# Optimization experiments

Measured on AMD Instinct MI355X. Metric: run time of the kernel, lower is better.

The kernel has to match this reference:

```python
import jax, jax.numpy as jnp
import numpy as np
import math

B, S, D, H = 4, 512, 1024, 16
DH = D // H
DQ = D // 4
MIN_STEPS, MAX_STEPS = 4, 12
THR = 1e-4


def lin(t, w, b):
    # torch Linear convention: w is (out, in)
    return jnp.einsum('...i,oi->...o', t, w) + b


def gelu(t):
    return jax.nn.gelu(t, approximate=False)  # torch nn.GELU() exact


def layernorm(t, g, b):
    m = t.mean(-1, keepdims=True)
    v = jnp.mean(jnp.square(t - m), axis=-1, keepdims=True)
    return (t - m) * jax.lax.rsqrt(v + 1e-5) * g + b


def _forward(h, x, ig_w1, ig_b1, ig_w2, ig_b2, wq, bq, wk, bk, wv, bv, wo, bo,
             g1_w1, g1_b1, g1_w2, g1_b2, gate_logits, ln_g, ln_b,
             sp_w1, sp_b1, sp_w2, sp_b2):
    # adaptive step count: steps = base + floor(sigmoid(MLP(mean_pool(h))).mean() * extra)
    pooled = h.mean(axis=1)  # (B, D)
    extra = jax.nn.sigmoid(lin(gelu(lin(pooled, sp_w1, sp_b1)), sp_w2, sp_b2)).mean()
    num_steps = jnp.minimum(
        MIN_STEPS + jnp.floor(extra * (MAX_STEPS - MIN_STEPS)).astype(jnp.int32), MAX_STEPS)

    gw = jax.nn.softmax(gate_logits)  # gate weights over the 3 gates
    scale = 1.0 / math.sqrt(DH)

    def step(carry, i):
        h, active = carry
        # G1 gate (G2/G3 multiply zero memory/expert outputs -> drop)
        G1 = jax.nn.sigmoid(lin(gelu(lin(h, g1_w1, g1_b1)), g1_w2, g1_b2)) * gw[0]
        # Phi: input-gated blend + raw multi-head self-attention
        gate = jax.nn.sigmoid(
            lin(gelu(lin(jnp.concatenate([h, x], axis=-1), ig_w1, ig_b1)), ig_w2, ig_b2))
        blended = gate * h + (1.0 - gate) * x
        q = lin(blended, wq, bq).reshape(B, S, H, DH)
        k = lin(blended, wk, bk).reshape(B, S, H, DH)
        v = lin(blended, wv, bv).reshape(B, S, H, DH)
        attn = jax.nn.softmax(jnp.einsum('bqhd,bkhd->bhqk', q, k) * scale, axis=-1)
        ctx = jnp.einsum('bhqk,bkhd->bqhd', attn, v).reshape(B, S, D)
        phi = lin(ctx, wo, bo)
        h_new = layernorm(h + G1 * phi, ln_g, ln_b)
        res = jnp.linalg.norm(h_new - h) / (jnp.linalg.norm(h) + 1e-8)
        act_i = active & (i < num_steps)
        h = jnp.where(act_i, h_new, h)
        active = act_i & jnp.logical_not((i >= MIN_STEPS) & (res < THR))
        return (h, active), None

    (h, _), _ = jax.lax.scan(step, (h, jnp.array(True)), jnp.arange(MAX_STEPS))
    return h


def setup_inputs() -> dict:
    key = jax.random.key(0)
    ks = jax.random.split(key, 16)
    f32 = jnp.float32

    def W(k, out_d, in_d):
        return jax.random.normal(k, (out_d, in_d), f32) * (1.0 / np.sqrt(in_d))

    return {
        'h': jax.random.normal(ks[0], (B, S, D), f32),
        'x': jax.random.normal(ks[1], (B, S, D), f32),
        # PhiLayer input_gate: Linear(2D, D/4) -> GELU -> Linear(D/4, D) -> Sigmoid
        'ig_w1': W(ks[2], DQ, 2 * D), 'ig_b1': jnp.zeros((DQ,), f32),
        'ig_w2': W(ks[3], D, DQ), 'ig_b2': jnp.zeros((D,), f32),
        # QKV / out projections (xavier-ish, zero bias)
        'wq': W(ks[4], D, D), 'bq': jnp.zeros((D,), f32),
        'wk': W(ks[5], D, D), 'bk': jnp.zeros((D,), f32),
        'wv': W(ks[6], D, D), 'bv': jnp.zeros((D,), f32),
        'wo': W(ks[7], D, D), 'bo': jnp.zeros((D,), f32),
        # Gating gate #1 MLP (only G1 contributes; memory/experts are zero)
        'g1_w1': W(ks[8], DQ, D), 'g1_b1': jnp.zeros((DQ,), f32),
        'g1_w2': W(ks[9], D, DQ), 'g1_b2': jnp.zeros((D,), f32),
        'gate_logits': jnp.ones((3,), f32),  # nn.Parameter(torch.ones(3))
        # LayerNorm
        'ln_g': jnp.ones((D,), f32), 'ln_b': jnp.zeros((D,), f32),
        # step predictor: Linear(D, D/4) -> GELU -> Linear(D/4, 1)
        'sp_w1': W(ks[10], DQ, D), 'sp_b1': jnp.zeros((DQ,), f32),
        'sp_w2': W(ks[11], 1, DQ), 'sp_b2': jnp.zeros((1,), f32),
    }


def reference(h, x, ig_w1, ig_b1, ig_w2, ig_b2, wq, bq, wk, bk, wv, bv, wo, bo,
              g1_w1, g1_b1, g1_w2, g1_b2, gate_logits, ln_g, ln_b,
              sp_w1, sp_b1, sp_w2, sp_b2):
    return _forward(h, x, ig_w1, ig_b1, ig_w2, ig_b2, wq, bq, wk, bk, wv, bv, wo, bo,
                    g1_w1, g1_b1, g1_w2, g1_b2, gate_logits, ln_g, ln_b,
                    sp_w1, sp_b1, sp_w2, sp_b2)
```

## Files before the change

### kernel.cpp

```cpp
#include <hip/hip_runtime.h>
#include <hip/hip_bf16.h>


#define B_   4
#define S_   512
#define D_   1024
#define H_   16
#define DH_  64
#define MSEQ 2048

typedef short short8 __attribute__((ext_vector_type(8)));
typedef float floatx4 __attribute__((ext_vector_type(4)));

static constexpr size_t OFF_H    = 0;
static constexpr size_t OFF_X    = 2097152;
static constexpr size_t OFF_HXB  = 4194304;
static constexpr size_t OFF_T2B  = 6291456;
static constexpr size_t OFF_T1B  = 6553600;
static constexpr size_t OFF_G1B  = 6815744;
static constexpr size_t OFF_QKVB = 7864320;
static constexpr size_t OFF_U    = 7864320;
static constexpr size_t OFF_CTXB = 11010048;
static constexpr size_t OFF_WARE = 12058624;
static constexpr size_t OFF_BIAS = 14811136;
static constexpr size_t OFF_POOL = 14817792;
static constexpr size_t OFF_SPT  = 14821888;
static constexpr size_t OFF_PPART= 14822912;
static constexpr size_t OFF_SCAL = 14888448;

static constexpr int W_WIG1 = 0;
static constexpr int W_WIG2 = 524288;
static constexpr int W_WG1  = 786432;
static constexpr int W_WG2  = 1048576;
static constexpr int W_QKV  = 1310720;
static constexpr int W_WO   = 4456448;
static constexpr int W_TOT  = 5505024;
static constexpr int B_TOT  = 6656;

__device__ __forceinline__ float bf2f(unsigned int u) {
  return __uint_as_float((u & 0xFFFFu) << 16);
}
__device__ __forceinline__ short f2bs(float f) {
  __hip_bfloat16 b = __float2bfloat16(f);
  return *reinterpret_cast<short*>(&b);
}
__device__ __forceinline__ unsigned int pk2(float lo, float hi) {
  return (unsigned int)(unsigned short)f2bs(lo) | ((unsigned int)(unsigned short)f2bs(hi) << 16);
}
__device__ __forceinline__ float ldf(const void* p, size_t i, int f32m) {
  return f32m ? ((const float*)p)[i] : bf2f(((const unsigned short*)p)[i]);
}
__device__ __forceinline__ float gelu_f(float x) {
  return 0.5f * x * (1.0f + erff(x * 0.70710678118654752440f));
}
__device__ __forceinline__ float sig_f(float x) {
  return 1.0f / (1.0f + expf(-x));
}
__device__ __forceinline__ void gl_lds16(const short* gp, short* lp) {
  __builtin_amdgcn_global_load_lds(
      (const __attribute__((address_space(1))) unsigned int*)gp,
      (__attribute__((address_space(3))) unsigned int*)lp, 16, 0, 0);
}
__device__ __forceinline__ float wave_sum(float v) {
  #pragma unroll
  for (int off = 32; off > 0; off >>= 1) v += __shfl_xor(v, off);
  return v;
}

__global__ void detect_kernel(const void* ln_g, int* dtf) {
  *dtf = (((const unsigned int*)ln_g)[0] == 0x3F800000u) ? 1 : 0;
}

struct RepackPtrs {
  const void* w[8];
  const void* b[8];
};

__global__ __launch_bounds__(256) void repack_all_kernel(
    const int* __restrict__ dtf, RepackPtrs ps,
    short* __restrict__ wdst, float* __restrict__ bdst) {
  const int f32m = *dtf;
  int i = blockIdx.x * 256 + threadIdx.x;
  if (i < W_TOT) {
    const int off[9] = {0, 524288, 786432, 1048576, 1310720, 2359296, 3407872, 4456448, W_TOT};
    int seg = 0;
    #pragma unroll
    for (int s = 1; s < 8; s++) seg += (i >= off[s]) ? 1 : 0;
    wdst[i] = f2bs(ldf(ps.w[seg], i - off[seg], f32m));
  } else if (i < W_TOT + B_TOT) {
    int j = i - W_TOT;
    const int off[9] = {0, 256, 1280, 1536, 2560, 3584, 4608, 5632, B_TOT};
    int seg = 0;
    #pragma unroll
    for (int s = 1; s < 8; s++) seg += (j >= off[s]) ? 1 : 0;
    bdst[j] = ldf(ps.b[seg], j - off[seg], f32m);
  }
}

__global__ __launch_bounds__(256) void cvt_in_kernel(
    const int* __restrict__ dtf, const void* __restrict__ hb,
    const void* __restrict__ xb, float* __restrict__ h, float* __restrict__ x,
    short* __restrict__ hxb, int n) {
  int f32m = *dtf;
  int i = blockIdx.x * 256 + threadIdx.x;
  if (i < n) {
    float hv = ldf(hb, i, f32m);
    float xv = ldf(xb, i, f32m);
    h[i] = hv;
    x[i] = xv;
    int row = i >> 10, col = i & 1023;
    hxb[(size_t)row * 2048 + col] = f2bs(hv);
    hxb[(size_t)row * 2048 + 1024 + col] = f2bs(xv);
  }
}

__global__ __launch_bounds__(256) void cvt_out_kernel(
    const int* __restrict__ dtf, const float* __restrict__ h, void* __restrict__ out, int n) {
  int f32m = *dtf;
  int i = blockIdx.x * 256 + threadIdx.x;
  if (i < n) {
    if (f32m) ((float*)out)[i] = h[i];
    else ((__hip_bfloat16*)out)[i] = __float2bfloat16(h[i]);
  }
}

__global__ __launch_bounds__(256) void pool_s1_kernel(
    const float* __restrict__ H, float* __restrict__ part) {
  int b = blockIdx.x, c = blockIdx.y, tid = threadIdx.x;
  const float* p = H + ((size_t)b * S_ + c * 32) * D_;
  #pragma unroll
  for (int rep = 0; rep < 4; rep++) {
    int d = rep * 256 + tid;
    float s = 0.f;
    for (int r = 0; r < 32; r++) s += p[(size_t)r * D_ + d];
    part[((size_t)b * 16 + c) * D_ + d] = s;
  }
}
__global__ __launch_bounds__(256) void pool_s2_kernel(
    const float* __restrict__ part, float* __restrict__ pooled) {
  int i = blockIdx.x * 256 + threadIdx.x;
  int b = i >> 10, d = i & 1023;
  float s = 0.f;
  #pragma unroll
  for (int c = 0; c < 16; c++) s += part[((size_t)b * 16 + c) * D_ + d];
  pooled[i] = s * (1.0f / (float)S_);
}

__device__ __forceinline__ float blk_sum256(float v, float* sm, int tid) {
  #pragma unroll
  for (int off = 32; off > 0; off >>= 1) v += __shfl_xor(v, off);
  __syncthreads();
  if ((tid & 63) == 0) sm[tid >> 6] = v;
  __syncthreads();
  return sm[0] + sm[1] + sm[2] + sm[3];
}

__global__ __launch_bounds__(256) void sp1_kernel(
    const int* __restrict__ dtf, const float* __restrict__ pooled,
    const void* __restrict__ w1, const void* __restrict__ b1,
    float* __restrict__ spt) {
  __shared__ float sm[4];
  const int f32m = *dtf;
  int j = blockIdx.x, tid = threadIdx.x;
  float s[4] = {0.f, 0.f, 0.f, 0.f};
  #pragma unroll
  for (int r = 0; r < 4; r++) {
    int k = tid * 4 + r;
    float w = ldf(w1, (size_t)j * D_ + k, f32m);
    s[0] += pooled[k] * w;
    s[1] += pooled[1024 + k] * w;
    s[2] += pooled[2048 + k] * w;
    s[3] += pooled[3072 + k] * w;
  }
  #pragma unroll
  for (int b = 0; b < 4; b++) {
    float t = blk_sum256(s[b], sm, tid);
    __syncthreads();
    if (tid == 0) spt[b * 256 + j] = gelu_f(t + ldf(b1, j, f32m));
  }
}

__global__ __launch_bounds__(256) void sp2_kernel(
    const int* __restrict__ dtf, const float* __restrict__ spt,
    const void* __restrict__ w2, const void* __restrict__ b2,
    const void* __restrict__ glog,
    int* __restrict__ num_steps, int* __restrict__ active, int* __restrict__ cur,
    float* __restrict__ gw0, float* __restrict__ ssd, float* __restrict__ ssh,
    int* __restrict__ cnt) {
  __shared__ float z[4];
  const int f32m = *dtf;
  int tid = threadIdx.x;
  if (tid < 12) cnt[tid] = 0;
  int wave = tid >> 6, lane = tid & 63;
  {
    int b = wave;
    float s = spt[b * 256 + lane]       * ldf(w2, lane, f32m) +
              spt[b * 256 + lane + 64]  * ldf(w2, lane + 64, f32m) +
              spt[b * 256 + lane + 128] * ldf(w2, lane + 128, f32m) +
              spt[b * 256 + lane + 192] * ldf(w2, lane + 192, f32m);
    #pragma unroll
    for (int off = 32; off > 0; off >>= 1) s += __shfl_xor(s, off);
    if (lane == 0) z[b] = sig_f(s + ldf(b2, 0, f32m));
  }
  __syncthreads();
  if (tid == 0) {
    float extra = 0.25f * (z[0] + z[1] + z[2] + z[3]);
    int ns = 4 + (int)floorf(extra * 8.0f);
    if (ns > 12) ns = 12;
    *num_steps = ns;
    *active = 1;
    *cur = 1;
    *ssd = 0.f; *ssh = 0.f;
    float g0 = ldf(glog, 0, f32m);
    float g1 = ldf(glog, 1, f32m);
    float g2 = ldf(glog, 2, f32m);
    float mx = fmaxf(g0, fmaxf(g1, g2));
    float e0 = expf(g0 - mx), e1 = expf(g1 - mx), e2 = expf(g2 - mx);
    *gw0 = e0 / (e0 + e1 + e2);
  }
}

enum { EPI_NONE = 0, EPI_GELU = 1, EPI_SIGSCALE = 2, EPI_BLEND = 3, EPI_RESADD = 4 };

template <int EPI, int BM, int BN>
__device__ __forceinline__ void mgemm_core(
    short* As, short* Bs,
    const short* __restrict__ A, int lda,
    const short* __restrict__ W, const float* __restrict__ bias, int K, int N,
    float* __restrict__ Cf, short* __restrict__ Cb,
    const float* __restrict__ aux1, const float* __restrict__ aux2f,
    const short* __restrict__ aux2b, const float* __restrict__ scale_ptr,
    int m0, int n0) {
  constexpr int FM = (BM / 2) / 16;
  constexpr int FN = (BN / 2) / 16;
  constexpr int CPA = (BM / 16) / 4;
  constexpr int CPB = (BN / 16) / 4;
  const int tid = threadIdx.x;
  const int lane = tid & 63, wv_ = tid >> 6;
  const int wm = (wv_ >> 1) * (BM / 2), wn = (wv_ & 1) * (BN / 2);
  const int srow = lane >> 2, scol = (lane & 3) * 8;
  const int frow = lane & 15, fk = (lane >> 4) * 8;

  floatx4 acc[FM][FN];
  #pragma unroll
  for (int i = 0; i < FM; i++)
    #pragma unroll
    for (int j = 0; j < FN; j++) acc[i][j] = (floatx4){0.f, 0.f, 0.f, 0.f};

  for (int k0 = 0; k0 < K; k0 += 64) {
    __syncthreads();
    #pragma unroll
    for (int c = 0; c < CPA; c++) {
      int q = wv_ * CPA + c;
      const short* gp = A + (size_t)(m0 + q * 16 + srow) * lda + k0 + scol;
      gl_lds16(gp, As + q * 512);
      gl_lds16(gp + 32, As + BM * 32 + q * 512);
    }
    #pragma unroll
    for (int c = 0; c < CPB; c++) {
      int q = wv_ * CPB + c;
      const short* gp = W + (size_t)(n0 + q * 16 + srow) * K + k0 + scol;
      gl_lds16(gp, Bs + q * 512);
      gl_lds16(gp + 32, Bs + BN * 32 + q * 512);
    }
    __syncthreads();
    #pragma unroll
    for (int hlf = 0; hlf < 2; hlf++) {
      const short* Ah = As + hlf * BM * 32;
      const short* Bh = Bs + hlf * BN * 32;
      short8 a[FM], b[FN];
      #pragma unroll
      for (int i = 0; i < FM; i++)
        a[i] = *reinterpret_cast<const short8*>(&Ah[(wm + i * 16 + frow) * 32 + fk]);
      #pragma unroll
      for (int j = 0; j < FN; j++)
        b[j] = *reinterpret_cast<const short8*>(&Bh[(wn + j * 16 + frow) * 32 + fk]);
      #pragma unroll
      for (int i = 0; i < FM; i++)
        #pragma unroll
        for (int j = 0; j < FN; j++)
          acc[i][j] = __builtin_amdgcn_mfma_f32_16x16x32_bf16(a[i], b[j], acc[i][j], 0, 0, 0);
    }
  }

  float gwv = 0.f;
  if (EPI == EPI_SIGSCALE) gwv = *scale_ptr;
  const int rq = (lane >> 4) * 4;
  #pragma unroll
  for (int i = 0; i < FM; i++) {
    #pragma unroll
    for (int j = 0; j < FN; j++) {
      int n = n0 + wn + j * 16 + (lane & 15);
      float bv = bias[n];
      #pragma unroll
      for (int r = 0; r < 4; r++) {
        int m = m0 + wm + i * 16 + rq + r;
        size_t off = (size_t)m * N + n;
        float v = acc[i][j][r] + bv;
        if (EPI == EPI_GELU) {
          Cb[off] = f2bs(gelu_f(v));
        } else if (EPI == EPI_SIGSCALE) {
          Cb[off] = f2bs(sig_f(v) * gwv);
        } else if (EPI == EPI_BLEND) {
          float s = sig_f(v);
          Cb[off] = f2bs(s * aux1[off] + (1.f - s) * aux2f[off]);
        } else if (EPI == EPI_RESADD) {
          Cf[off] = aux1[off] + bf2f((unsigned short)aux2b[off]) * v;
        } else {
          Cb[off] = f2bs(v);
        }
      }
    }
  }
}

template <int EPI, int BM, int BN>
__global__ __launch_bounds__(256) void mgemm(
    const int* __restrict__ flag, const short* __restrict__ A, int lda,
    const short* __restrict__ W, const float* __restrict__ bias, int K, int N,
    float* __restrict__ Cf, short* __restrict__ Cb,
    const float* __restrict__ aux1, const float* __restrict__ aux2f,
    const short* __restrict__ aux2b, const float* __restrict__ scale_ptr) {
  if (*flag == 0) return;
  __shared__ short As[BM * 64];
  __shared__ short Bs[BN * 64];
  mgemm_core<EPI, BM, BN>(As, Bs, A, lda, W, bias, K, N, Cf, Cb,
                          aux1, aux2f, aux2b, scale_ptr,
                          blockIdx.y * BM, blockIdx.x * BN);
}

__global__ __launch_bounds__(256) void gate1_kernel(
    const int* __restrict__ flag, const short* __restrict__ hxb,
    const short* __restrict__ warena, const float* __restrict__ biasA,
    short* __restrict__ t2b, short* __restrict__ t1b) {
  if (*flag == 0) return;
  __shared__ short As[64 * 64];
  __shared__ short Bs[64 * 64];
  if (blockIdx.z == 0)
    mgemm_core<EPI_GELU, 64, 64>(As, Bs, hxb, 2048, warena + W_WIG1, biasA + 0,
                                 2048, 256, nullptr, t2b, nullptr, nullptr, nullptr,
                                 nullptr, blockIdx.y * 64, blockIdx.x * 64);
  else
    mgemm_core<EPI_GELU, 64, 64>(As, Bs, hxb, 2048, warena + W_WG1, biasA + 1280,
                                 1024, 256, nullptr, t1b, nullptr, nullptr, nullptr,
                                 nullptr, blockIdx.y * 64, blockIdx.x * 64);
}

__global__ __launch_bounds__(256) void gate2_kernel(
    const int* __restrict__ flag, const short* __restrict__ t2b,
    const short* __restrict__ t1b, const short* __restrict__ warena,
    const float* __restrict__ biasA, short* __restrict__ bldb,
    short* __restrict__ g1b, const float* __restrict__ h,
    const float* __restrict__ xf, const float* __restrict__ gw0) {
  if (*flag == 0) return;
  __shared__ short As[128 * 64];
  __shared__ short Bs[64 * 64];
  if (blockIdx.z == 0)
    mgemm_core<EPI_BLEND, 128, 64>(As, Bs, t2b, 256, warena + W_WIG2, biasA + 256,
                                   256, 1024, nullptr, bldb, h, xf, nullptr,
                                   nullptr, blockIdx.y * 128, blockIdx.x * 64);
  else
    mgemm_core<EPI_SIGSCALE, 128, 64>(As, Bs, t1b, 256, warena + W_WG2, biasA + 1536,
                                      256, 1024, nullptr, g1b, nullptr, nullptr,
                                      nullptr, gw0, blockIdx.y * 128, blockIdx.x * 64);
}

#define AP_ 72
__global__ __launch_bounds__(256) void attn_kernel(
    const int* __restrict__ flag, const short* __restrict__ qkv,
    short* __restrict__ ctxb) {
  if (*flag == 0) return;
  __shared__ short Ks[64 * AP_];
  __shared__ short Vt[64 * AP_];
  __shared__ short Ps[64 * AP_];
  const int tid = threadIdx.x;
  const int lane = tid & 63, wv = tid >> 6;
  const int ln15 = lane & 15, quad = lane >> 4;
  const int qt = blockIdx.x, hh = blockIdx.y, b = blockIdx.z;
  const int wm = wv * 16;
  const size_t rowbase = (size_t)b * S_;
  const int hcol = hh * DH_;
  const float scale = 0.125f;

  short8 qa[2];
  {
    const short* qp = qkv + (rowbase + qt * 64 + wm + ln15) * 3072 + hcol + quad * 8;
    qa[0] = *reinterpret_cast<const short8*>(qp);
    qa[1] = *reinterpret_cast<const short8*>(qp + 32);
  }
  const int skk = tid >> 2, scg = (tid & 3) * 16;

  float mrow[4] = {-1e30f, -1e30f, -1e30f, -1e30f};
  float lrow[4] = {0.f, 0.f, 0.f, 0.f};
  floatx4 accO[4];
  #pragma unroll
  for (int j = 0; j < 4; j++) accO[j] = (floatx4){0.f, 0.f, 0.f, 0.f};

  for (int kt = 0; kt < 8; kt++) {
    __syncthreads();
    {
      const short* gk = qkv + (rowbase + kt * 64 + skk) * 3072 + 1024 + hcol + scg;
      uint4 k0 = *reinterpret_cast<const uint4*>(gk);
      uint4 k1 = *reinterpret_cast<const uint4*>(gk + 8);
      *reinterpret_cast<uint4*>(&Ks[skk * AP_ + scg]) = k0;
      *reinterpret_cast<uint4*>(&Ks[skk * AP_ + scg + 8]) = k1;
      short8 v0 = *reinterpret_cast<const short8*>(gk + 1024);
      short8 v1 = *reinterpret_cast<const short8*>(gk + 1032);
      #pragma unroll
      for (int j = 0; j < 8; j++) Vt[(scg + j) * AP_ + skk] = v0[j];
      #pragma unroll
      for (int j = 0; j < 8; j++) Vt[(scg + 8 + j) * AP_ + skk] = v1[j];
    }
    __syncthreads();

    floatx4 sc[4];
    #pragma unroll
    for (int nf = 0; nf < 4; nf++) {
      short8 b0 = *reinterpret_cast<const short8*>(&Ks[(nf * 16 + ln15) * AP_ + quad * 8]);
      short8 b1 = *reinterpret_cast<const short8*>(&Ks[(nf * 16 + ln15) * AP_ + 32 + quad * 8]);
      floatx4 s = (floatx4){0.f, 0.f, 0.f, 0.f};
      s = __builtin_amdgcn_mfma_f32_16x16x32_bf16(qa[0], b0, s, 0, 0, 0);
      s = __builtin_amdgcn_mfma_f32_16x16x32_bf16(qa[1], b1, s, 0, 0, 0);
      sc[nf] = s;
    }

    float prob[4][4];
    #pragma unroll
    for (int r = 0; r < 4; r++) {
      float lm = fmaxf(fmaxf(sc[0][r], sc[1][r]), fmaxf(sc[2][r], sc[3][r])) * scale;
      lm = fmaxf(lm, __shfl_xor(lm, 1));
      lm = fmaxf(lm, __shfl_xor(lm, 2));
      lm = fmaxf(lm, __shfl_xor(lm, 4));
      lm = fmaxf(lm, __shfl_xor(lm, 8));
      float mn = fmaxf(mrow[r], lm);
      float alpha = expf(mrow[r] - mn);
      float ls = 0.f;
      #pragma unroll
      for (int nf = 0; nf < 4; nf++) {
        float p = expf(sc[nf][r] * scale - mn);
        prob[nf][r] = p;
        ls += p;
      }
      ls += __shfl_xor(ls, 1);
      ls += __shfl_xor(ls, 2);
      ls += __shfl_xor(ls, 4);
      ls += __shfl_xor(ls, 8);
      lrow[r] = lrow[r] * alpha + ls;
      mrow[r] = mn;
      #pragma unroll
      for (int df = 0; df < 4; df++) accO[df][r] *= alpha;
    }
    #pragma unroll
    for (int nf = 0; nf < 4; nf++)
      #pragma unroll
      for (int r = 0; r < 4; r++)
        Ps[(wm + quad * 4 + r) * AP_ + nf * 16 + ln15] = f2bs(prob[nf][r]);
    __syncthreads();

    short8 pa0 = *reinterpret_cast<const short8*>(&Ps[(wm + ln15) * AP_ + quad * 8]);
    short8 pa1 = *reinterpret_cast<const short8*>(&Ps[(wm + ln15) * AP_ + 32 + quad * 8]);
    #pragma unroll
    for (int df = 0; df < 4; df++) {
      short8 bv0 = *reinterpret_cast<const short8*>(&Vt[(df * 16 + ln15) * AP_ + quad * 8]);
      short8 bv1 = *reinterpret_cast<const short8*>(&Vt[(df * 16 + ln15) * AP_ + 32 + quad * 8]);
      accO[df] = __builtin_amdgcn_mfma_f32_16x16x32_bf16(pa0, bv0, accO[df], 0, 0, 0);
      accO[df] = __builtin_amdgcn_mfma_f32_16x16x32_bf16(pa1, bv1, accO[df], 0, 0, 0);
    }
  }

  float inv[4];
  #pragma unroll
  for (int r = 0; r < 4; r++) inv[r] = 1.0f / lrow[r];
  #pragma unroll
  for (int df = 0; df < 4; df++) {
    #pragma unroll
    for (int r = 0; r < 4; r++) {
      size_t off = (rowbase + qt * 64 + wm + quad * 4 + r) * 1024 + hcol + df * 16 + ln15;
      ctxb[off] = f2bs(accO[df][r] * inv[r]);
    }
  }
}

__global__ __launch_bounds__(256) void ln_kernel(
    int step_i, const int* __restrict__ flagp, const int* __restrict__ dtf,
    const float* __restrict__ U, float* __restrict__ H, short* __restrict__ hxb,
    const void* __restrict__ g, const void* __restrict__ be,
    float* __restrict__ ssd, float* __restrict__ ssh,
    int* __restrict__ active, int* __restrict__ cur,
    const int* __restrict__ num_steps, int* __restrict__ cnt) {
  const int flag = *flagp;
  const int f32m = *dtf;
  __shared__ float sdd[4], sdh[4];
  const int tid = threadIdx.x;
  const int wv = tid >> 6, lane = tid & 63;
  if (flag) {
    const int row = blockIdx.x * 4 + wv;
    const float4* u4 = reinterpret_cast<const float4*>(U + (size_t)row * D_);
    float4* h4 = reinterpret_cast<float4*>(H + (size_t)row * D_);
    float4 uv[4], hv[4];
    #pragma unroll
    for (int j = 0; j < 4; j++) uv[j] = u4[lane + 64 * j];
    #pragma unroll
    for (int j = 0; j < 4; j++) hv[j] = h4[lane + 64 * j];
    float s = 0.f;
    #pragma unroll
    for (int j = 0; j < 4; j++) s += (uv[j].x + uv[j].y) + (uv[j].z + uv[j].w);
    s = wave_sum(s);
    float mean = s * (1.0f / (float)D_);
    float4 d[4];
    float vv = 0.f;
    #pragma unroll
    for (int j = 0; j < 4; j++) {
      d[j].x = uv[j].x - mean; d[j].y = uv[j].y - mean;
      d[j].z = uv[j].z - mean; d[j].w = uv[j].w - mean;
      vv += d[j].x * d[j].x + d[j].y * d[j].y + d[j].z * d[j].z + d[j].w * d[j].w;
    }
    vv = wave_sum(vv);
    float rstd = rsqrtf(vv * (1.0f / (float)D_) + 1e-5f);
    float lsd = 0.f, lsh = 0.f;
    #pragma unroll
    for (int j = 0; j < 4; j++) {
      int c = (lane + 64 * j) * 4;
      float hn0 = d[j].x * rstd * ldf(g, c + 0, f32m) + ldf(be, c + 0, f32m);
      float hn1 = d[j].y * rstd * ldf(g, c + 1, f32m) + ldf(be, c + 1, f32m);
      float hn2 = d[j].z * rstd * ldf(g, c + 2, f32m) + ldf(be, c + 2, f32m);
      float hn3 = d[j].w * rstd * ldf(g, c + 3, f32m) + ldf(be, c + 3, f32m);
      float e0 = hn0 - hv[j].x, e1 = hn1 - hv[j].y, e2 = hn2 - hv[j].z, e3 = hn3 - hv[j].w;
      lsd += e0 * e0 + e1 * e1 + e2 * e2 + e3 * e3;
      lsh += hv[j].x * hv[j].x + hv[j].y * hv[j].y + hv[j].z * hv[j].z + hv[j].w * hv[j].w;
      h4[lane + 64 * j] = make_float4(hn0, hn1, hn2, hn3);
      uint2 pw;
      pw.x = pk2(hn0, hn1);
      pw.y = pk2(hn2, hn3);
      *reinterpret_cast<uint2*>(hxb + (size_t)row * 2048 + c) = pw;
    }
    lsd = wave_sum(lsd);
    lsh = wave_sum(lsh);
    if (lane == 0) { sdd[wv] = lsd; sdh[wv] = lsh; }
    __syncthreads();
    if (tid == 0) {
      atomicAdd(ssd, (sdd[0] + sdd[1]) + (sdd[2] + sdd[3]));
      atomicAdd(ssh, (sdh[0] + sdh[1]) + (sdh[2] + sdh[3]));
    }
  }
  if (tid == 0) {
    __threadfence();
    int old = atomicAdd(&cnt[step_i], 1);
    if (old == (int)gridDim.x - 1) {
      if (flag && step_i >= 4) {
        float nd = atomicAdd(ssd, 0.0f);
        float nh = atomicAdd(ssh, 0.0f);
        float res = sqrtf(nd) / (sqrtf(nh) + 1e-8f);
        if (res < 1e-4f) *active = 0;
      }
      *cur = ((*active) && (step_i + 1 < *num_steps)) ? 1 : 0;
      *ssd = 0.f; *ssh = 0.f;
    }
  }
}

extern "C" void kernel_launch(void* const* d_in, const int* in_sizes, int n_in,
                              void* d_out, int out_size, void* d_ws, size_t ws_size,
                              hipStream_t stream) {
  (void)in_sizes; (void)n_in; (void)out_size; (void)ws_size;
  const void* h_in  = d_in[0];
  const void* x_in  = d_in[1];
  const void* glog  = d_in[18];
  const void* ln_g  = d_in[19];
  const void* ln_b  = d_in[20];
  const void* sp_w1 = d_in[21];
  const void* sp_b1 = d_in[22];
  const void* sp_w2 = d_in[23];
  const void* sp_b2 = d_in[24];

  RepackPtrs rp;
  rp.w[0] = d_in[2];  rp.w[1] = d_in[4];  rp.w[2] = d_in[14]; rp.w[3] = d_in[16];
  rp.w[4] = d_in[6];  rp.w[5] = d_in[8];  rp.w[6] = d_in[10]; rp.w[7] = d_in[12];
  rp.b[0] = d_in[3];  rp.b[1] = d_in[5];  rp.b[2] = d_in[15]; rp.b[3] = d_in[17];
  rp.b[4] = d_in[7];  rp.b[5] = d_in[9];  rp.b[6] = d_in[11]; rp.b[7] = d_in[13];

  float* wsf = (float*)d_ws;
  float* h      = wsf + OFF_H;
  float* xf     = wsf + OFF_X;
  short* hxb    = (short*)(wsf + OFF_HXB);
  short* t2b    = (short*)(wsf + OFF_T2B);
  short* t1b    = (short*)(wsf + OFF_T1B);
  short* g1b    = (short*)(wsf + OFF_G1B);
  short* qkvb   = (short*)(wsf + OFF_QKVB);
  float* u      = wsf + OFF_U;
  short* ctxb   = (short*)(wsf + OFF_CTXB);
  short* bldb   = ctxb;
  short* warena = (short*)(wsf + OFF_WARE);
  float* biasA  = wsf + OFF_BIAS;
  float* pooled = wsf + OFF_POOL;
  float* spt    = wsf + OFF_SPT;
  float* ppart  = wsf + OFF_PPART;
  float* ssd    = wsf + OFF_SCAL + 0;
  float* ssh    = wsf + OFF_SCAL + 1;
  float* gw0    = wsf + OFF_SCAL + 2;
  int* ip        = (int*)(wsf + OFF_SCAL + 8);
  int* num_steps = ip + 0;
  int* active    = ip + 1;
  int* cur       = ip + 2;
  int* dtf       = ip + 3;
  int* cnt       = ip + 4;

  const int NTOT = B_ * S_ * D_;

  detect_kernel<<<1, 1, 0, stream>>>(ln_g, dtf);
  repack_all_kernel<<<(W_TOT + B_TOT + 255) / 256, 256, 0, stream>>>(dtf, rp, warena, biasA);
  cvt_in_kernel<<<NTOT / 256, 256, 0, stream>>>(dtf, h_in, x_in, h, xf, hxb, NTOT);
  pool_s1_kernel<<<dim3(4, 16), 256, 0, stream>>>(h, ppart);
  pool_s2_kernel<<<16, 256, 0, stream>>>(ppart, pooled);
  sp1_kernel<<<256, 256, 0, stream>>>(dtf, pooled, sp_w1, sp_b1, spt);
  sp2_kernel<<<1, 256, 0, stream>>>(dtf, spt, sp_w2, sp_b2, glog,
                                    num_steps, active, cur, gw0, ssd, ssh, cnt);
  for (int i = 0; i < 12; i++) {
    gate1_kernel<<<dim3(4, 32, 2), 256, 0, stream>>>(cur, hxb, warena, biasA, t2b, t1b);
    gate2_kernel<<<dim3(16, 16, 2), 256, 0, stream>>>(cur, t2b, t1b, warena, biasA,
                                                      bldb, g1b, h, xf, gw0);
    mgemm<EPI_NONE, 128, 64><<<dim3(48, 16), 256, 0, stream>>>(
        cur, bldb, 1024, warena + W_QKV, biasA + 2560, 1024, 3072,
        nullptr, qkvb, nullptr, nullptr, nullptr, nullptr);
    attn_kernel<<<dim3(8, 16, 4), 256, 0, stream>>>(cur, qkvb, ctxb);
    mgemm<EPI_RESADD, 128, 64><<<dim3(16, 16), 256, 0, stream>>>(
        cur, ctxb, 1024, warena + W_WO, biasA + 5632, 1024, 1024,
        u, nullptr, h, nullptr, g1b, nullptr);
    ln_kernel<<<512, 256, 0, stream>>>(i, cur, dtf, u, h, hxb, ln_g, ln_b,
                                       ssd, ssh, active, cur, num_steps, cnt);
  }
  cvt_out_kernel<<<NTOT / 256, 256, 0, stream>>>(dtf, h, (void*)d_out, NTOT);
}
```

Baseline: 1.275 ms.

## Fuse per-step kernels into persistent megakernel with grid barriers and early exit

Replaces the 12-iteration loop of six kernel launches per step (gate1, gate2, QKV GEMM, attention, output GEMM, layernorm) with one persistent kernel of 512 blocks. The stages are separated by a software grid barrier built on an atomic counter, and the kernel breaks out of the loop once the step count or convergence test says to stop. This removes launch overhead and the no-op launches that ran after convergence, and the output conversion is folded into the kernel's tail. The cost is spin-wait barriers, which only work if all 512 blocks are co-resident and would deadlock otherwise. Per-step residual accumulators replace reset logic, and stages with fewer work items than blocks leave some blocks idle.

After: 3.858 ms. 203% more time.

```diff
diff --git a/kernel.cpp b/kernel.cpp
--- a/kernel.cpp
+++ b/kernel.cpp
@@ -8,6 +8,7 @@
 #define H_   16
 #define DH_  64
 #define MSEQ 2048
+#define NBLK 512
 
 typedef short short8 __attribute__((ext_vector_type(8)));
 typedef float floatx4 __attribute__((ext_vector_type(4)));
@@ -67,6 +68,20 @@
   return v;
 }
 
+__device__ __forceinline__ void gbar(int* bar, int& nbar) {
+  __syncthreads();
+  if (threadIdx.x == 0) {
+    __threadfence();
+    __hip_atomic_fetch_add(bar, 1, __ATOMIC_RELAXED, __HIP_MEMORY_SCOPE_AGENT);
+    const int target = NBLK * (nbar + 1);
+    while (__hip_atomic_load(bar, __ATOMIC_RELAXED, __HIP_MEMORY_SCOPE_AGENT) < target)
+      __builtin_amdgcn_s_sleep(2);
+    __threadfence();
+  }
+  __syncthreads();
+  nbar++;
+}
+
 __global__ void detect_kernel(const void* ln_g, int* dtf) {
   *dtf = (((const unsigned int*)ln_g)[0] == 0x3F800000u) ? 1 : 0;
 }
@@ -114,16 +129,6 @@
   }
 }
 
-__global__ __launch_bounds__(256) void cvt_out_kernel(
-    const int* __restrict__ dtf, const float* __restrict__ h, void* __restrict__ out, int n) {
-  int f32m = *dtf;
-  int i = blockIdx.x * 256 + threadIdx.x;
-  if (i < n) {
-    if (f32m) ((float*)out)[i] = h[i];
-    else ((__hip_bfloat16*)out)[i] = __float2bfloat16(h[i]);
-  }
-}
-
 __global__ __launch_bounds__(256) void pool_s1_kernel(
     const float* __restrict__ H, float* __restrict__ part) {
   int b = blockIdx.x, c = blockIdx.y, tid = threadIdx.x;
@@ -184,13 +189,13 @@
     const int* __restrict__ dtf, const float* __restrict__ spt,
     const void* __restrict__ w2, const void* __restrict__ b2,
     const void* __restrict__ glog,
-    int* __restrict__ num_steps, int* __restrict__ active, int* __restrict__ cur,
-    float* __restrict__ gw0, float* __restrict__ ssd, float* __restrict__ ssh,
-    int* __restrict__ cnt) {
+    int* __restrict__ num_steps, float* __restrict__ gw0,
+    float* __restrict__ ssdA, float* __restrict__ sshA, int* __restrict__ bar) {
   __shared__ float z[4];
   const int f32m = *dtf;
   int tid = threadIdx.x;
-  if (tid < 12) cnt[tid] = 0;
+  if (tid < 12) { ssdA[tid] = 0.f; sshA[tid] = 0.f; }
+  if (tid == 16) *bar = 0;
   int wave = tid >> 6, lane = tid & 63;
   {
     int b = wave;
@@ -208,9 +213,6 @@
     int ns = 4 + (int)floorf(extra * 8.0f);
     if (ns > 12) ns = 12;
     *num_steps = ns;
-    *active = 1;
-    *cur = 1;
-    *ssd = 0.f; *ssh = 0.f;
     float g0 = ldf(glog, 0, f32m);
     float g1 = ldf(glog, 1, f32m);
     float g2 = ldf(glog, 2, f32m);
@@ -314,69 +316,16 @@
   }
 }
 
-template <int EPI, int BM, int BN>
-__global__ __launch_bounds__(256) void mgemm(
-    const int* __restrict__ flag, const short* __restrict__ A, int lda,
-    const short* __restrict__ W, const float* __restrict__ bias, int K, int N,
-    float* __restrict__ Cf, short* __restrict__ Cb,
-    const float* __restrict__ aux1, const float* __restrict__ aux2f,
-    const short* __restrict__ aux2b, const float* __restrict__ scale_ptr) {
-  if (*flag == 0) return;
-  __shared__ short As[BM * 64];
-  __shared__ short Bs[BN * 64];
-  mgemm_core<EPI, BM, BN>(As, Bs, A, lda, W, bias, K, N, Cf, Cb,
-                          aux1, aux2f, aux2b, scale_ptr,
-                          blockIdx.y * BM, blockIdx.x * BN);
-}
-
-__global__ __launch_bounds__(256) void gate1_kernel(
-    const int* __restrict__ flag, const short* __restrict__ hxb,
-    const short* __restrict__ warena, const float* __restrict__ biasA,
-    short* __restrict__ t2b, short* __restrict__ t1b) {
-  if (*flag == 0) return;
-  __shared__ short As[64 * 64];
-  __shared__ short Bs[64 * 64];
-  if (blockIdx.z == 0)
-    mgemm_core<EPI_GELU, 64, 64>(As, Bs, hxb, 2048, warena + W_WIG1, biasA + 0,
-                                 2048, 256, nullptr, t2b, nullptr, nullptr, nullptr,
-                                 nullptr, blockIdx.y * 64, blockIdx.x * 64);
-  else
-    mgemm_core<EPI_GELU, 64, 64>(As, Bs, hxb, 2048, warena + W_WG1, biasA + 1280,
-                                 1024, 256, nullptr, t1b, nullptr, nullptr, nullptr,
-                                 nullptr, blockIdx.y * 64, blockIdx.x * 64);
-}
-
-__global__ __launch_bounds__(256) void gate2_kernel(
-    const int* __restrict__ flag, const short* __restrict__ t2b,
-    const short* __restrict__ t1b, const short* __restrict__ warena,
-    const float* __restrict__ biasA, short* __restrict__ bldb,
-    short* __restrict__ g1b, const float* __restrict__ h,
-    const float* __restrict__ xf, const float* __restrict__ gw0) {
-  if (*flag == 0) return;
-  __shared__ short As[128 * 64];
-  __shared__ short Bs[64 * 64];
-  if (blockIdx.z == 0)
-    mgemm_core<EPI_BLEND, 128, 64>(As, Bs, t2b, 256, warena + W_WIG2, biasA + 256,
-                                   256, 1024, nullptr, bldb, h, xf, nullptr,
-                                   nullptr, blockIdx.y * 128, blockIdx.x * 64);
-  else
-    mgemm_core<EPI_SIGSCALE, 128, 64>(As, Bs, t1b, 256, warena + W_WG2, biasA + 1536,
-                                      256, 1024, nullptr, g1b, nullptr, nullptr,
-                                      nullptr, gw0, blockIdx.y * 128, blockIdx.x * 64);
-}
-
 #define AP_ 72
-__global__ __launch_bounds__(256) void attn_kernel(
-    const int* __restrict__ flag, const short* __restrict__ qkv,
-    short* __restrict__ ctxb) {
-  if (*flag == 0) return;
-  __shared__ short Ks[64 * AP_];
-  __shared__ short Vt[64 * AP_];
-  __shared__ short Ps[64 * AP_];
+__device__ __forceinline__ void attn_core(
+    short* smem, const short* __restrict__ qkv, short* __restrict__ ctxb, int item) {
+  short* Ks = smem;
+  short* Vt = smem + 64 * AP_;
+  short* Ps = smem + 2 * 64 * AP_;
   const int tid = threadIdx.x;
   const int lane = tid & 63, wv = tid >> 6;
   const int ln15 = lane & 15, quad = lane >> 4;
-  const int qt = blockIdx.x, hh = blockIdx.y, b = blockIdx.z;
+  const int qt = item & 7, hh = (item >> 3) & 15, b = item >> 7;
   const int wm = wv * 16;
   const size_t rowbase = (size_t)b * S_;
   const int hcol = hh * DH_;
@@ -481,80 +430,145 @@
   }
 }
 
-__global__ __launch_bounds__(256) void ln_kernel(
-    int step_i, const int* __restrict__ flagp, const int* __restrict__ dtf,
-    const float* __restrict__ U, float* __restrict__ H, short* __restrict__ hxb,
-    const void* __restrict__ g, const void* __restrict__ be,
-    float* __restrict__ ssd, float* __restrict__ ssh,
-    int* __restrict__ active, int* __restrict__ cur,
-    const int* __restrict__ num_steps, int* __restrict__ cnt) {
-  const int flag = *flagp;
-  const int f32m = *dtf;
-  __shared__ float sdd[4], sdh[4];
+__device__ __forceinline__ void ln_core(
+    int f32m, const float* __restrict__ U, float* __restrict__ H,
+    short* __restrict__ hxb, const void* __restrict__ g, const void* __restrict__ be,
+    float* __restrict__ ssd, float* __restrict__ ssh, float* sred, int item) {
   const int tid = threadIdx.x;
   const int wv = tid >> 6, lane = tid & 63;
-  if (flag) {
-    const int row = blockIdx.x * 4 + wv;
-    const float4* u4 = reinterpret_cast<const float4*>(U + (size_t)row * D_);
-    float4* h4 = reinterpret_cast<float4*>(H + (size_t)row * D_);
-    float4 uv[4], hv[4];
-    #pragma unroll
-    for (int j = 0; j < 4; j++) uv[j] = u4[lane + 64 * j];
-    #pragma unroll
-    for (int j = 0; j < 4; j++) hv[j] = h4[lane + 64 * j];
-    float s = 0.f;
-    #pragma unroll
-    for (int j = 0; j < 4; j++) s += (uv[j].x + uv[j].y) + (uv[j].z + uv[j].w);
-    s = wave_sum(s);
-    float mean = s * (1.0f / (float)D_);
-    float4 d[4];
-    float vv = 0.f;
-    #pragma unroll
-    for (int j = 0; j < 4; j++) {
-      d[j].x = uv[j].x - mean; d[j].y = uv[j].y - mean;
-      d[j].z = uv[j].z - mean; d[j].w = uv[j].w - mean;
-      vv += d[j].x * d[j].x + d[j].y * d[j].y + d[j].z * d[j].z + d[j].w * d[j].w;
-    }
-    vv = wave_sum(vv);
-    float rstd = rsqrtf(vv * (1.0f / (float)D_) + 1e-5f);
-    float lsd = 0.f, lsh = 0.f;
-    #pragma unroll
-    for (int j = 0; j < 4; j++) {
-      int c = (lane + 64 * j) * 4;
-      float hn0 = d[j].x * rstd * ldf(g, c + 0, f32m) + ldf(be, c + 0, f32m);
-      float hn1 = d[j].y * rstd * ldf(g, c + 1, f32m) + ldf(be, c + 1, f32m);
-      float hn2 = d[j].z * rstd * ldf(g, c + 2, f32m) + ldf(be, c + 2, f32m);
-      float hn3 = d[j].w * rstd * ldf(g, c + 3, f32m) + ldf(be, c + 3, f32m);
-      float e0 = hn0 - hv[j].x, e1 = hn1 - hv[j].y, e2 = hn2 - hv[j].z, e3 = hn3 - hv[j].w;
-      lsd += e0 * e0 + e1 * e1 + e2 * e2 + e3 * e3;
-      lsh += hv[j].x * hv[j].x + hv[j].y * hv[j].y + hv[j].z * hv[j].z + hv[j].w * hv[j].w;
-      h4[lane + 64 * j] = make_float4(hn0, hn1, hn2, hn3);
-      uint2 pw;
-      pw.x = pk2(hn0, hn1);
-      pw.y = pk2(hn2, hn3);
-      *reinterpret_cast<uint2*>(hxb + (size_t)row * 2048 + c) = pw;
-    }
-    lsd = wave_sum(lsd);
-    lsh = wave_sum(lsh);
-    if (lane == 0) { sdd[wv] = lsd; sdh[wv] = lsh; }
-    __syncthreads();
-    if (tid == 0) {
-      atomicAdd(ssd, (sdd[0] + sdd[1]) + (sdd[2] + sdd[3]));
-      atomicAdd(ssh, (sdh[0] + sdh[1]) + (sdh[2] + sdh[3]));
-    }
-  }
+  const int row = item * 4 + wv;
+  const float4* u4 = reinterpret_cast<const float4*>(U + (size_t)row * D_);
+  float4* h4 = reinterpret_cast<float4*>(H + (size_t)row * D_);
+  float4 uv[4], hv[4];
+  #pragma unroll
+  for (int j = 0; j < 4; j++) uv[j] = u4[lane + 64 * j];
+  #pragma unroll
+  for (int j = 0; j < 4; j++) hv[j] = h4[lane + 64 * j];
+  float s = 0.f;
+  #pragma unroll
+  for (int j = 0; j < 4; j++) s += (uv[j].x + uv[j].y) + (uv[j].z + uv[j].w);
+  s = wave_sum(s);
+  float mean = s * (1.0f / (float)D_);
+  float4 d[4];
+  float vv = 0.f;
+  #pragma unroll
+  for (int j = 0; j < 4; j++) {
+    d[j].x = uv[j].x - mean; d[j].y = uv[j].y - mean;
+    d[j].z = uv[j].z - mean; d[j].w = uv[j].w - mean;
+    vv += d[j].x * d[j].x + d[j].y * d[j].y + d[j].z * d[j].z + d[j].w * d[j].w;
+  }
+  vv = wave_sum(vv);
+  float rstd = rsqrtf(vv * (1.0f / (float)D_) + 1e-5f);
+  float lsd = 0.f, lsh = 0.f;
+  #pragma unroll
+  for (int j = 0; j < 4; j++) {
+    int c = (lane + 64 * j) * 4;
+    float hn0 = d[j].x * rstd * ldf(g, c + 0, f32m) + ldf(be, c + 0, f32m);
+    float hn1 = d[j].y * rstd * ldf(g, c + 1, f32m) + ldf(be, c + 1, f32m);
+    float hn2 = d[j].z * rstd * ldf(g, c + 2, f32m) + ldf(be, c + 2, f32m);
+    float hn3 = d[j].w * rstd * ldf(g, c + 3, f32m) + ldf(be, c + 3, f32m);
+    float e0 = hn0 - hv[j].x, e1 = hn1 - hv[j].y, e2 = hn2 - hv[j].z, e3 = hn3 - hv[j].w;
+    lsd += e0 * e0 + e1 * e1 + e2 * e2 + e3 * e3;
+    lsh += hv[j].x * hv[j].x + hv[j].y * hv[j].y + hv[j].z * hv[j].z + hv[j].w * hv[j].w;
+    h4[lane + 64 * j] = make_float4(hn0, hn1, hn2, hn3);
+    uint2 pw;
+    pw.x = pk2(hn0, hn1);
+    pw.y = pk2(hn2, hn3);
+    *reinterpret_cast<uint2*>(hxb + (size_t)row * 2048 + c) = pw;
+  }
+  lsd = wave_sum(lsd);
+  lsh = wave_sum(lsh);
+  if (lane == 0) { sred[wv] = lsd; sred[4 + wv] = lsh; }
+  __syncthreads();
   if (tid == 0) {
-    __threadfence();
-    int old = atomicAdd(&cnt[step_i], 1);
-    if (old == (int)gridDim.x - 1) {
-      if (flag && step_i >= 4) {
-        float nd = atomicAdd(ssd, 0.0f);
-        float nh = atomicAdd(ssh, 0.0f);
-        float res = sqrtf(nd) / (sqrtf(nh) + 1e-8f);
-        if (res < 1e-4f) *active = 0;
-      }
-      *cur = ((*active) && (step_i + 1 < *num_steps)) ? 1 : 0;
-      *ssd = 0.f; *ssh = 0.f;
+    atomicAdd(ssd, (sred[0] + sred[1]) + (sred[2] + sred[3]));
+    atomicAdd(ssh, (sred[4] + sred[5]) + (sred[6] + sred[7]));
+  }
+}
+
+__global__ __launch_bounds__(256, 2) void mega_kernel(
+    const int* __restrict__ dtf, const short* __restrict__ hxb_c, short* __restrict__ hxb,
+    const short* __restrict__ warena, const float* __restrict__ biasA,
+    short* __restrict__ t2b, short* __restrict__ t1b, short* __restrict__ g1b,
+    short* __restrict__ qkvb, float* __restrict__ u, short* __restrict__ ctxb,
+    float* __restrict__ h, const float* __restrict__ xf,
+    const void* __restrict__ ln_g, const void* __restrict__ ln_b,
+    float* __restrict__ ssdA, float* __restrict__ sshA,
+    const float* __restrict__ gw0, const int* __restrict__ num_steps,
+    int* __restrict__ bar, void* __restrict__ out) {
+  __shared__ short smem[64 * AP_ * 3];
+  __shared__ float sred[8];
+  const int f32m = *dtf;
+  const int nsL = *num_steps;
+  const int bid = blockIdx.x;
+  short* bldb = ctxb;
+  int activeL = 1;
+  int nbar = 0;
+
+  for (int step = 0; step < 12; step++) {
+    for (int it = bid; it < 256; it += NBLK) {
+      int z = it >> 7, rem = it & 127;
+      int my = rem & 31, nx = rem >> 5;
+      if (z == 0)
+        mgemm_core<EPI_GELU, 64, 64>(smem, smem + 4096, hxb_c, 2048, warena + W_WIG1,
+            biasA + 0, 2048, 256, nullptr, t2b, nullptr, nullptr, nullptr, nullptr,
+            my * 64, nx * 64);
+      else
+        mgemm_core<EPI_GELU, 64, 64>(smem, smem + 4096, hxb_c, 2048, warena + W_WG1,
+            biasA + 1280, 1024, 256, nullptr, t1b, nullptr, nullptr, nullptr, nullptr,
+            my * 64, nx * 64);
+    }
+    gbar(bar, nbar);
+    {
+      int z = bid >> 8, rem = bid & 255;
+      int my = rem & 15, nx = rem >> 4;
+      if (z == 0)
+        mgemm_core<EPI_BLEND, 128, 64>(smem, smem + 8192, t2b, 256, warena + W_WIG2,
+            biasA + 256, 256, 1024, nullptr, bldb, h, xf, nullptr, nullptr,
+            my * 128, nx * 64);
+      else
+        mgemm_core<EPI_SIGSCALE, 128, 64>(smem, smem + 8192, t1b, 256, warena + W_WG2,
+            biasA + 1536, 256, 1024, nullptr, g1b, nullptr, nullptr, nullptr, gw0,
+            my * 128, nx * 64);
+    }
+    gbar(bar, nbar);
+    for (int it = bid; it < 768; it += NBLK) {
+      int nx = it % 48, my = it / 48;
+      mgemm_core<EPI_NONE, 128, 64>(smem, smem + 8192, bldb, 1024, warena + W_QKV,
+          biasA + 2560, 1024, 3072, nullptr, qkvb, nullptr, nullptr, nullptr, nullptr,
+          my * 128, nx * 64);
+    }
+    gbar(bar, nbar);
+    attn_core(smem, qkvb, ctxb, bid);
+    gbar(bar, nbar);
+    for (int it = bid; it < 256; it += NBLK) {
+      int nx = it & 15, my = it >> 4;
+      mgemm_core<EPI_RESADD, 128, 64>(smem, smem + 8192, ctxb, 1024, warena + W_WO,
+          biasA + 5632, 1024, 1024, u, nullptr, h, nullptr, g1b, nullptr,
+          my * 128, nx * 64);
+    }
+    gbar(bar, nbar);
+    ln_core(f32m, u, h, hxb, ln_g, ln_b, &ssdA[step], &sshA[step], sred, bid);
+    gbar(bar, nbar);
+    if (step >= 4) {
+      float nd = __hip_atomic_load(&ssdA[step], __ATOMIC_RELAXED, __HIP_MEMORY_SCOPE_AGENT);
+      float nh = __hip_atomic_load(&sshA[step], __ATOMIC_RELAXED, __HIP_MEMORY_SCOPE_AGENT);
+      float res = sqrtf(nd) / (sqrtf(nh) + 1e-8f);
+      if (res < 1e-4f) activeL = 0;
+    }
+    if (!(activeL && (step + 1 < nsL))) break;
+  }
+
+  {
+    int base = bid * 4096 + threadIdx.x;
+    if (f32m) {
+      float* o = (float*)out;
+      #pragma unroll
+      for (int r = 0; r < 16; r++) o[base + r * 256] = h[base + r * 256];
+    } else {
+      __hip_bfloat16* o = (__hip_bfloat16*)out;
+      #pragma unroll
+      for (int r = 0; r < 16; r++) o[base + r * 256] = __float2bfloat16(h[base + r * 256]);
     }
   }
 }
@@ -589,21 +603,18 @@
   short* qkvb   = (short*)(wsf + OFF_QKVB);
   float* u      = wsf + OFF_U;
   short* ctxb   = (short*)(wsf + OFF_CTXB);
-  short* bldb   = ctxb;
   short* warena = (short*)(wsf + OFF_WARE);
   float* biasA  = wsf + OFF_BIAS;
   float* pooled = wsf + OFF_POOL;
   float* spt    = wsf + OFF_SPT;
   float* ppart  = wsf + OFF_PPART;
-  float* ssd    = wsf + OFF_SCAL + 0;
-  float* ssh    = wsf + OFF_SCAL + 1;
-  float* gw0    = wsf + OFF_SCAL + 2;
-  int* ip        = (int*)(wsf + OFF_SCAL + 8);
+  float* ssdA   = wsf + OFF_SCAL;
+  float* sshA   = wsf + OFF_SCAL + 12;
+  float* gw0    = wsf + OFF_SCAL + 24;
+  int* ip        = (int*)(wsf + OFF_SCAL + 28);
   int* num_steps = ip + 0;
-  int* active    = ip + 1;
-  int* cur       = ip + 2;
-  int* dtf       = ip + 3;
-  int* cnt       = ip + 4;
+  int* dtf       = ip + 1;
+  int* bar       = ip + 2;
 
   const int NTOT = B_ * S_ * D_;
 
@@ -614,20 +625,8 @@
   pool_s2_kernel<<<16, 256, 0, stream>>>(ppart, pooled);
   sp1_kernel<<<256, 256, 0, stream>>>(dtf, pooled, sp_w1, sp_b1, spt);
   sp2_kernel<<<1, 256, 0, stream>>>(dtf, spt, sp_w2, sp_b2, glog,
-                                    num_steps, active, cur, gw0, ssd, ssh, cnt);
-  for (int i = 0; i < 12; i++) {
-    gate1_kernel<<<dim3(4, 32, 2), 256, 0, stream>>>(cur, hxb, warena, biasA, t2b, t1b);
-    gate2_kernel<<<dim3(16, 16, 2), 256, 0, stream>>>(cur, t2b, t1b, warena, biasA,
-                                                      bldb, g1b, h, xf, gw0);
-    mgemm<EPI_NONE, 128, 64><<<dim3(48, 16), 256, 0, stream>>>(
-        cur, bldb, 1024, warena + W_QKV, biasA + 2560, 1024, 3072,
-        nullptr, qkvb, nullptr, nullptr, nullptr, nullptr);
-    attn_kernel<<<dim3(8, 16, 4), 256, 0, stream>>>(cur, qkvb, ctxb);
-    mgemm<EPI_RESADD, 128, 64><<<dim3(16, 16), 256, 0, stream>>>(
-        cur, ctxb, 1024, warena + W_WO, biasA + 5632, 1024, 1024,
-        u, nullptr, h, nullptr, g1b, nullptr);
-    ln_kernel<<<512, 256, 0, stream>>>(i, cur, dtf, u, h, hxb, ln_g, ln_b,
-                                       ssd, ssh, active, cur, num_steps, cnt);
-  }
-  cvt_out_kernel<<<NTOT / 256, 256, 0, stream>>>(dtf, h, (void*)d_out, NTOT);
-}
+                                    num_steps, gw0, ssdA, sshA, bar);
+  mega_kernel<<<NBLK, 256, 0, stream>>>(
+      dtf, hxb, hxb, warena, biasA, t2b, t1b, g1b, qkvb, u, ctxb,
+      h, xf, ln_g, ln_b, ssdA, sshA, gw0, num_steps, bar, d_out);
+}
```
